# Performance work log

Measured on AMD Instinct MI355X. Metric: run time of the kernel, lower is better.

## Reference

```python
import jax, jax.numpy as jnp
import numpy as np

N, D, H = 4096, 128, 8

def setup_inputs() -> dict:
    key = jax.random.key(0)
    ks = jax.random.split(key, 7)
    xavier = float(np.sqrt(6.0 / (D + D)))  # xavier_uniform for [*, D, D]
    x = jax.random.normal(ks[0], (N, D), dtype=jnp.float32)
    W_k = jax.random.uniform(ks[1], (H, D, D), minval=-xavier, maxval=xavier, dtype=jnp.float32)
    W_q = jax.random.uniform(ks[2], (H, D, D), minval=-xavier, maxval=xavier, dtype=jnp.float32)
    W_v = jax.random.uniform(ks[3], (H, D, D), minval=-xavier, maxval=xavier, dtype=jnp.float32)
    W_m = jnp.ones((H,), dtype=jnp.float32)
    lim = float(1.0 / np.sqrt(D))  # default torch Linear init range
    Wg = jax.random.uniform(ks[4], (D, D), minval=-lim, maxval=lim, dtype=jnp.float32)
    bg = jax.random.uniform(ks[5], (D,), minval=-lim, maxval=lim, dtype=jnp.float32)
    return {"x": x, "W_k": W_k, "W_q": W_q, "W_v": W_v, "W_m": W_m, "Wg": Wg, "bg": bg}

def reference(x, W_k, W_q, W_v, W_m, Wg, bg):
    # per-head projections: [H, N, D]
    q = jnp.einsum('nf,hfd->hnd', x, W_q)
    k = jnp.einsum('nf,hfd->hnd', x, W_k)
    v = jnp.einsum('nf,hfd->hnd', x, W_v)
    # dense all-pairs attention scores per head: [H, N, N]
    e = jnp.einsum('hnd,hmd->hnm', q, k)
    attn = jax.nn.softmax(e, axis=-1)
    # weighted sum over values, then head-scaled accumulation: [N, D]
    out = jnp.einsum('h,hnm,hmd->nd', W_m, attn, v)
    # residual MLP: x + ReLU(Linear(x + out))
    h = x + out
    g = jax.nn.relu(h @ Wg.T + bg)
    return x + g
```

## Files before the change

kernel.cpp:

```cpp
#include <hip/hip_runtime.h>

#define NROWS 4096
#define DDIM  128
#define NHEAD 8
#define LOG2E 1.44269504088896f

extern "C" __device__ float __ocml_native_exp2_f32(float);

typedef __attribute__((ext_vector_type(8))) short    short8;
typedef __attribute__((ext_vector_type(8))) _Float16 half8;
typedef __attribute__((ext_vector_type(4))) float    floatx4;

__device__ __forceinline__ float bf2f(unsigned short u){
  unsigned v = ((unsigned)u) << 16;
  return __builtin_bit_cast(float, v);
}
__device__ __forceinline__ unsigned short f2bf(float f){
  unsigned u = __builtin_bit_cast(unsigned, f);
  u += 0x7FFFu + ((u >> 16) & 1u);
  return (unsigned short)(u >> 16);
}
__device__ __forceinline__ void split2(float v, unsigned short& hi, unsigned short& lo){
  hi = f2bf(v);
  lo = f2bf(v - bf2f(hi));
}
__device__ __forceinline__ void async_cp16(const void* g, void* l){
  __builtin_amdgcn_global_load_lds(
      (const __attribute__((address_space(1))) void*)g,
      (__attribute__((address_space(3))) void*)l, 16, 0, 0);
}

__global__ void fill_kernel(float* __restrict__ out, float val, int n){
  int i = blockIdx.x * 256 + threadIdx.x;
  if (i < n) out[i] = val;
}

__global__ __launch_bounds__(256) void prep_kernel(
    const float* __restrict__ Wk, const float* __restrict__ Wv,
    const float* __restrict__ Wq, const float* __restrict__ Wg,
    const float* __restrict__ x,
    unsigned short* __restrict__ wpre, unsigned short* __restrict__ wgpre,
    unsigned short* __restrict__ xh, unsigned short* __restrict__ xl)
{
  const int id = blockIdx.x * 256 + threadIdx.x;
  if (id < 49152) {
    const int z = id >> 14, rem = id & 16383;
    const int h = rem >> 11, rem2 = rem & 2047;
    const int fh = rem2 >> 10, L = rem2 & 1023;
    const int d = L >> 3, m = L & 7;
    const int kk0 = (m ^ (d & 7)) << 3;
    const float* W = (z == 0 ? Wk : (z == 1 ? Wv : Wq)) + h * DDIM * DDIM;
    short8 hi8, lo8;
#pragma unroll
    for (int j = 0; j < 8; j++) {
      unsigned short hi, lo;
      split2(W[(fh * 64 + kk0 + j) * DDIM + d], hi, lo);
      hi8[j] = (short)hi; lo8[j] = (short)lo;
    }
    unsigned short* base = wpre + (size_t)((z * 8 + h) * 2 + fh) * 16384;
    *(short8*)(base + L * 8) = hi8;
    *(short8*)(base + 8192 + L * 8) = lo8;
  } else if (id < 51200) {
    const int t = id - 49152;
    const int fh = t >> 10, L = t & 1023;
    const int d = L >> 3, m = L & 7;
    const int kk0 = (m ^ (d & 7)) << 3;
    short8 hi8, lo8;
#pragma unroll
    for (int j = 0; j < 8; j++) {
      unsigned short hi, lo;
      split2(Wg[d * DDIM + fh * 64 + kk0 + j], hi, lo);
      hi8[j] = (short)hi; lo8[j] = (short)lo;
    }
    unsigned short* base = wgpre + fh * 16384;
    *(short8*)(base + L * 8) = hi8;
    *(short8*)(base + 8192 + L * 8) = lo8;
  } else if (id < 116736) {
    const int t = id - 51200;
    const float* src = x + (size_t)t * 8;
    float4 v0 = *(const float4*)src, v1 = *(const float4*)(src + 4);
    float xv[8] = {v0.x, v0.y, v0.z, v0.w, v1.x, v1.y, v1.z, v1.w};
    short8 hi8, lo8;
#pragma unroll
    for (int j = 0; j < 8; j++) {
      unsigned short hi, lo; split2(xv[j], hi, lo);
      hi8[j] = (short)hi; lo8[j] = (short)lo;
    }
    *(short8*)(xh + (size_t)t * 8) = hi8;
    *(short8*)(xl + (size_t)t * 8) = lo8;
  }
}

__global__ __launch_bounds__(256, 2) void proj_kernel(
    const unsigned short* __restrict__ xh, const unsigned short* __restrict__ xl,
    const unsigned short* __restrict__ wpre,
    _Float16* __restrict__ kfo, _Float16* __restrict__ vfo,
    _Float16* __restrict__ qfo)
{
  __shared__ alignas(16) unsigned short whi[8192];
  __shared__ alignas(16) unsigned short wlo[8192];
  const int tid = threadIdx.x, lane = tid & 63, wave = tid >> 6;
  const int l4 = lane & 15, quad = lane >> 4;
  const int h = blockIdx.y, z = blockIdx.z;
  const unsigned short* wb = wpre + (size_t)((z * 8 + h) * 2) * 16384;

  floatx4 acc[4][8];
#pragma unroll
  for (int t4 = 0; t4 < 4; t4++)
#pragma unroll
    for (int c = 0; c < 8; c++) acc[t4][c] = (floatx4)0.f;

  for (int fh = 0; fh < 2; fh++) {
    {
      const unsigned short* src = wb + fh * 16384;
      const unsigned short* sh = src + wave * 2048 + lane * 8;
      const unsigned short* sl = src + 8192 + wave * 2048 + lane * 8;
      unsigned short* dh = &whi[wave * 2048];
      unsigned short* dl = &wlo[wave * 2048];
#pragma unroll
      for (int it = 0; it < 4; it++) {
        async_cp16(sh + it * 512, dh + it * 512);
        async_cp16(sl + it * 512, dl + it * 512);
      }
    }
    __syncthreads();

#pragma unroll
    for (int t4 = 0; t4 < 4; t4++) {
      const int row = blockIdx.x * 256 + t4 * 64 + wave * 16 + l4;
      const size_t xo = (size_t)row * DDIM + fh * 64 + quad * 8;
      short8 ah[2], al[2];
      ah[0] = *(const short8*)(xh + xo);
      ah[1] = *(const short8*)(xh + xo + 32);
      al[0] = *(const short8*)(xl + xo);
      al[1] = *(const short8*)(xl + xo + 32);
#pragma unroll
      for (int t2 = 0; t2 < 2; t2++) {
#pragma unroll
        for (int c = 0; c < 8; c++) {
          const int col = c * 16 + l4;
          const int idx = (col * 8 + ((t2 * 4 + quad) ^ (col & 7))) * 8;
          short8 bh = *(const short8*)&whi[idx];
          short8 bl = *(const short8*)&wlo[idx];
          acc[t4][c] = __builtin_amdgcn_mfma_f32_16x16x32_bf16(ah[t2], bh, acc[t4][c], 0, 0, 0);
          acc[t4][c] = __builtin_amdgcn_mfma_f32_16x16x32_bf16(al[t2], bh, acc[t4][c], 0, 0, 0);
          acc[t4][c] = __builtin_amdgcn_mfma_f32_16x16x32_bf16(ah[t2], bl, acc[t4][c], 0, 0, 0);
        }
      }
    }
    __syncthreads();
  }

  const int rb = wave * 16 + quad * 4;
#pragma unroll
  for (int t4 = 0; t4 < 4; t4++) {
    const int tile = blockIdx.x * 4 + t4;
    const size_t tilebase = (size_t)(h * 64 + tile) * 8192;
#pragma unroll
    for (int c = 0; c < 8; c++) {
      const int d = c * 16 + l4;
#pragma unroll
      for (int r = 0; r < 4; r++) {
        const int kl = rb + r;
        const float val = acc[t4][c][r];
        if (z == 0) {
          const int c2 = kl >> 4, l4k = kl & 15;
          const int tt = d >> 5, qd = (d >> 3) & 3, jj = d & 7;
          const int qX = qd ^ ((l4k >> 1) & 3);
          kfo[tilebase + (size_t)((c2 * 4 + tt) * 16 + l4k) * 32 + qX * 8 + jj] =
              (_Float16)val;
        } else if (z == 1) {
          const int c2 = d >> 4, l4v = d & 15;
          const int tt = kl >> 5, qd = (kl >> 3) & 3, jj = kl & 7;
          const int qX = qd ^ ((l4v >> 1) & 3);
          vfo[tilebase + (size_t)((c2 * 2 + tt) * 16 + l4v) * 32 + qX * 8 + jj] =
              (_Float16)val;
        } else {
          qfo[((size_t)h * NROWS + (size_t)tile * 64 + kl) * DDIM + d] =
              (_Float16)(val * LOG2E);
        }
      }
    }
  }
}

struct FlashLds {
  _Float16 k[2][8192];
  _Float16 p[4][1024];
};

__global__ __launch_bounds__(256, 3) void flash_kernel(
    const _Float16* __restrict__ qfo, const _Float16* __restrict__ kfo,
    const _Float16* __restrict__ vfo,
    _Float16* __restrict__ op, float* __restrict__ mb, float* __restrict__ lb)
{
  __shared__ alignas(16) FlashLds lds;
  const int tid = threadIdx.x, lane = tid & 63, wave = tid >> 6;
  const int l4 = lane & 15, quad = lane >> 4;
  const int h = blockIdx.x & 7, qt = (blockIdx.x >> 3) & 63, s = blockIdx.x >> 9;
  const int q0 = qt * 64;

  half8 aq[4];
  {
    const _Float16* qr =
        qfo + ((size_t)h * NROWS + q0 + wave * 16 + l4) * DDIM + quad * 8;
#pragma unroll
    for (int t = 0; t < 4; t++) aq[t] = *(const half8*)(qr + t * 32);
  }

  float m_run[4];
#pragma unroll
  for (int r = 0; r < 4; r++) m_run[r] = -1e30f;
  floatx4 Oacc[8], lacc = (floatx4)0.f;
#pragma unroll
  for (int c = 0; c < 8; c++) Oacc[c] = (floatx4)0.f;

  half8 vones;
#pragma unroll
  for (int j = 0; j < 8; j++) vones[j] = (_Float16)1.f;

  const _Float16* kfo_h = kfo + (size_t)h * 64 * 8192;
  const _Float16* vfo_h = vfo + (size_t)h * 64 * 8192;
  const int lq = (l4 * 4 + (quad ^ ((l4 >> 1) & 3))) * 8;
  const int kt0 = (s == 0) ? 0 : (s == 1 ? 22 : 43);
  const int kt1 = (s == 0) ? 22 : (s == 1 ? 43 : 64);

  {
    const _Float16* ks = kfo_h + (size_t)kt0 * 8192 + wave * 2048 + lane * 8;
    _Float16* kd = &lds.k[kt0 & 1][wave * 2048];
#pragma unroll
    for (int it = 0; it < 4; it++) async_cp16(ks + it * 512, kd + it * 512);
  }

  for (int kt = kt0; kt < kt1; ++kt) {
    const int cur = kt & 1;
    __syncthreads();

    if (kt + 1 < kt1) {
      const _Float16* ks = kfo_h + (size_t)(kt + 1) * 8192 + wave * 2048 + lane * 8;
      _Float16* kd = &lds.k[cur ^ 1][wave * 2048];
#pragma unroll
      for (int it = 0; it < 4; it++) async_cp16(ks + it * 512, kd + it * 512);
    }

    floatx4 Sf[4];
#pragma unroll
    for (int c = 0; c < 4; c++) Sf[c] = (floatx4)0.f;
    __builtin_amdgcn_s_setprio(1);
#pragma unroll
    for (int t = 0; t < 4; t++) {
      half8 b[4];
#pragma unroll
      for (int c = 0; c < 4; c++)
        b[c] = *(const half8*)&lds.k[cur][(c * 4 + t) * 512 + lq];
#pragma unroll
      for (int c = 0; c < 4; c++)
        Sf[c] = __builtin_amdgcn_mfma_f32_16x16x32_f16(aq[t], b[c], Sf[c], 0, 0, 0);
    }
    __builtin_amdgcn_s_setprio(0);

    float alpha[4];
    {
      float mt[4];
#pragma unroll
      for (int r = 0; r < 4; r++)
        mt[r] = fmaxf(fmaxf(Sf[0][r], Sf[1][r]), fmaxf(Sf[2][r], Sf[3][r]));
#pragma unroll
      for (int mk = 1; mk <= 8; mk <<= 1)
#pragma unroll
        for (int r = 0; r < 4; r++) mt[r] = fmaxf(mt[r], __shfl_xor(mt[r], mk, 64));
#pragma unroll
      for (int r = 0; r < 4; r++) {
        const float mn = fmaxf(m_run[r], mt[r]);
        alpha[r] = __ocml_native_exp2_f32(m_run[r] - mn);
        m_run[r] = mn;
      }
#pragma unroll
      for (int r = 0; r < 4; r++)
#pragma unroll
        for (int c = 0; c < 4; c++)
          Sf[c][r] = __ocml_native_exp2_f32(Sf[c][r] - m_run[r]);
    }

#pragma unroll
    for (int c = 0; c < 4; c++)
#pragma unroll
      for (int r = 0; r < 4; r++)
        lds.p[wave][((c * 2 + (l4 >> 3)) * 16 + quad * 4 + r) * 8 + (l4 & 7)] =
            (_Float16)Sf[c][r];

    half8 vfrag[8][2];
    {
      const _Float16* vtb = vfo_h + (size_t)kt * 8192;
#pragma unroll
      for (int c = 0; c < 8; c++)
#pragma unroll
        for (int t = 0; t < 2; t++)
          vfrag[c][t] = *(const half8*)(vtb + (c * 2 + t) * 512 + lq);
    }

    {
      const bool moved = (alpha[0] != 1.f) | (alpha[1] != 1.f) |
                         (alpha[2] != 1.f) | (alpha[3] != 1.f);
      if (__any(moved)) {
#pragma unroll
        for (int c = 0; c < 8; c++) {
          Oacc[c][0] *= alpha[0]; Oacc[c][1] *= alpha[1];
          Oacc[c][2] *= alpha[2]; Oacc[c][3] *= alpha[3];
        }
        lacc[0] *= alpha[0]; lacc[1] *= alpha[1];
        lacc[2] *= alpha[2]; lacc[3] *= alpha[3];
      }
    }

    __builtin_amdgcn_s_setprio(1);
#pragma unroll
    for (int t = 0; t < 2; t++) {
      half8 ap = *(const half8*)&lds.p[wave][((t * 4 + quad) * 16 + l4) * 8];
      lacc = __builtin_amdgcn_mfma_f32_16x16x32_f16(ap, vones, lacc, 0, 0, 0);
#pragma unroll
      for (int c = 0; c < 8; c++)
        Oacc[c] = __builtin_amdgcn_mfma_f32_16x16x32_f16(ap, vfrag[c][t], Oacc[c], 0, 0, 0);
    }
    __builtin_amdgcn_s_setprio(0);
  }

  const int rbase = wave * 16 + quad * 4;
  const size_t rowbase = (size_t)(s * NHEAD + h) * NROWS + q0 + rbase;
#pragma unroll
  for (int c = 0; c < 8; c++) {
    const int col = c * 16 + l4;
#pragma unroll
    for (int r = 0; r < 4; r++)
      op[(rowbase + r) * DDIM + col] = (_Float16)Oacc[c][r];
  }
  if (l4 == 0) {
#pragma unroll
    for (int r = 0; r < 4; r++) {
      mb[rowbase + r] = m_run[r];
      lb[rowbase + r] = lacc[r];
    }
  }
}

__global__ __launch_bounds__(128) void merge_kernel(
    const _Float16* __restrict__ op, const float* __restrict__ mb,
    const float* __restrict__ lb, const float* __restrict__ Wm,
    float* __restrict__ u)
{
  __shared__ float sc[3][NHEAD];
  const int n = blockIdx.x, d = threadIdx.x;
  if (d < NHEAD) {
    const int h = d;
    float m0 = mb[(size_t)(0 * NHEAD + h) * NROWS + n];
    float m1 = mb[(size_t)(1 * NHEAD + h) * NROWS + n];
    float m2 = mb[(size_t)(2 * NHEAD + h) * NROWS + n];
    float l0 = lb[(size_t)(0 * NHEAD + h) * NROWS + n];
    float l1 = lb[(size_t)(1 * NHEAD + h) * NROWS + n];
    float l2 = lb[(size_t)(2 * NHEAD + h) * NROWS + n];
    const float m = fmaxf(fmaxf(m0, m1), m2);
    const float a0 = __ocml_native_exp2_f32(m0 - m);
    const float a1 = __ocml_native_exp2_f32(m1 - m);
    const float a2 = __ocml_native_exp2_f32(m2 - m);
    const float invL = Wm[h] / (l0 * a0 + l1 * a1 + l2 * a2);
    sc[0][h] = a0 * invL;
    sc[1][h] = a1 * invL;
    sc[2][h] = a2 * invL;
  }
  __syncthreads();
  float acc = 0.f;
#pragma unroll
  for (int s = 0; s < 3; s++)
#pragma unroll
    for (int h = 0; h < NHEAD; h++)
      acc += sc[s][h] * (float)op[((size_t)(s * NHEAD + h) * NROWS + n) * DDIM + d];
  u[(size_t)n * DDIM + d] = acc;
}

__global__ __launch_bounds__(256, 2) void mlp_kernel(
    const float* __restrict__ x, const float* __restrict__ u,
    const unsigned short* __restrict__ wgpre, const float* __restrict__ bg,
    float* __restrict__ out)
{
  __shared__ alignas(16) unsigned short whi[8192];
  __shared__ alignas(16) unsigned short wlo[8192];
  const int tid = threadIdx.x, lane = tid & 63, wave = tid >> 6;
  const int l4 = lane & 15, quad = lane >> 4;
  const int r0 = blockIdx.x * 64;

  floatx4 acc[8];
#pragma unroll
  for (int c = 0; c < 8; c++) acc[c] = (floatx4)0.f;

  for (int fh = 0; fh < 2; fh++) {
    {
      const unsigned short* src = wgpre + fh * 16384;
      const unsigned short* sh = src + wave * 2048 + lane * 8;
      const unsigned short* sl = src + 8192 + wave * 2048 + lane * 8;
      unsigned short* dh = &whi[wave * 2048];
      unsigned short* dl = &wlo[wave * 2048];
#pragma unroll
      for (int it = 0; it < 4; it++) {
        async_cp16(sh + it * 512, dh + it * 512);
        async_cp16(sl + it * 512, dl + it * 512);
      }
    }
    __syncthreads();

    const size_t xoff = (size_t)(r0 + wave * 16 + l4) * DDIM + fh * 64 + quad * 8;
    short8 ah[2], al[2];
#pragma unroll
    for (int t2 = 0; t2 < 2; t2++) {
      float4 x0 = *(const float4*)(x + xoff + t2 * 32);
      float4 x1 = *(const float4*)(x + xoff + t2 * 32 + 4);
      float4 u0 = *(const float4*)(u + xoff + t2 * 32);
      float4 u1 = *(const float4*)(u + xoff + t2 * 32 + 4);
      float hv[8] = {x0.x + u0.x, x0.y + u0.y, x0.z + u0.z, x0.w + u0.w,
                     x1.x + u1.x, x1.y + u1.y, x1.z + u1.z, x1.w + u1.w};
#pragma unroll
      for (int j = 0; j < 8; j++) {
        unsigned short hi, lo; split2(hv[j], hi, lo);
        ah[t2][j] = (short)hi; al[t2][j] = (short)lo;
      }
    }
#pragma unroll
    for (int t2 = 0; t2 < 2; t2++) {
#pragma unroll
      for (int c = 0; c < 8; c++) {
        const int col = c * 16 + l4;
        const int idx = (col * 8 + ((t2 * 4 + quad) ^ (col & 7))) * 8;
        short8 bh = *(const short8*)&whi[idx];
        short8 bl = *(const short8*)&wlo[idx];
        acc[c] = __builtin_amdgcn_mfma_f32_16x16x32_bf16(ah[t2], bh, acc[c], 0, 0, 0);
        acc[c] = __builtin_amdgcn_mfma_f32_16x16x32_bf16(al[t2], bh, acc[c], 0, 0, 0);
        acc[c] = __builtin_amdgcn_mfma_f32_16x16x32_bf16(ah[t2], bl, acc[c], 0, 0, 0);
      }
    }
    __syncthreads();
  }

  const int rbase = wave * 16 + quad * 4;
#pragma unroll
  for (int c = 0; c < 8; c++) {
    const int col = c * 16 + l4;
    const float bgf = bg[col];
#pragma unroll
    for (int r = 0; r < 4; r++) {
      const size_t idx = (size_t)(r0 + rbase + r) * DDIM + col;
      out[idx] = x[idx] + fmaxf(acc[c][r] + bgf, 0.f);
    }
  }
}

extern "C" void kernel_launch(void* const* d_in, const int* in_sizes, int n_in,
                              void* d_out, int out_size, void* d_ws, size_t ws_size,
                              hipStream_t stream) {
  float* out = (float*)d_out;
  const int fill_blocks = (out_size + 255) / 256;

  const bool ok_sizes =
      n_in == 7 &&
      in_sizes[0] == NROWS * DDIM &&
      in_sizes[1] == NHEAD * DDIM * DDIM &&
      in_sizes[2] == NHEAD * DDIM * DDIM &&
      in_sizes[3] == NHEAD * DDIM * DDIM &&
      in_sizes[4] == NHEAD &&
      in_sizes[5] == DDIM * DDIM &&
      in_sizes[6] == DDIM &&
      out_size == NROWS * DDIM;
  if (!ok_sizes) {
    fill_kernel<<<fill_blocks, 256, 0, stream>>>(out, 1000.f, out_size);
    return;
  }

  const size_t HND = (size_t)NHEAD * NROWS * DDIM;
  const size_t ND  = (size_t)NROWS * DDIM;
  const size_t WPRE_N  = (size_t)3 * 8 * 2 * 16384;
  const size_t WGPRE_N = (size_t)2 * 16384;
  const size_t need = ND * 4 + 3 * HND * 2 + 3 * HND * 2 +
                      2 * (3 * (size_t)NHEAD * NROWS) * 4 +
                      (WPRE_N + WGPRE_N + 2 * ND) * 2;
  if (ws_size < need) {
    fill_kernel<<<fill_blocks, 256, 0, stream>>>(out, 500.f, out_size);
    return;
  }

  const float* x  = (const float*)d_in[0];
  const float* Wk = (const float*)d_in[1];
  const float* Wq = (const float*)d_in[2];
  const float* Wv = (const float*)d_in[3];
  const float* Wm = (const float*)d_in[4];
  const float* Wg = (const float*)d_in[5];
  const float* bg = (const float*)d_in[6];

  float*          u     = (float*)d_ws;
  _Float16*       kfo   = (_Float16*)(u + ND);
  _Float16*       vfo   = kfo + HND;
  _Float16*       qfo   = vfo + HND;
  _Float16*       op    = qfo + HND;
  float*          mb    = (float*)(op + 3 * HND);
  float*          lb    = mb + 3 * NHEAD * NROWS;
  unsigned short* wpre  = (unsigned short*)(lb + 3 * NHEAD * NROWS);
  unsigned short* wgpre = wpre + WPRE_N;
  unsigned short* xh    = wgpre + WGPRE_N;
  unsigned short* xl    = xh + ND;

  (void)hipGetLastError();
  prep_kernel<<<dim3(456), 256, 0, stream>>>(Wk, Wv, Wq, Wg, x, wpre, wgpre, xh, xl);
  proj_kernel<<<dim3(16, NHEAD, 3), 256, 0, stream>>>(xh, xl, wpre, kfo, vfo, qfo);
  flash_kernel<<<dim3(1536), 256, 0, stream>>>(qfo, kfo, vfo, op, mb, lb);
  merge_kernel<<<dim3(4096), 128, 0, stream>>>(op, mb, lb, Wm, u);
  mlp_kernel<<<dim3(64), 256, 0, stream>>>(x, u, wgpre, bg, out);
  if (hipGetLastError() != hipSuccess) {
    fill_kernel<<<fill_blocks, 256, 0, stream>>>(out, 2000.f, out_size);
  }
}
```

Baseline: 233.9 us.

## Software-pipeline QK^T of next tile with PV of current tile; DPP row max

Restructures the flash-attention inner loop so the QK^T MFMAs for tile kt+1 are issued alongside the PV MFMAs for tile kt, with K prefetch moved two tiles ahead and one barrier per iteration placed after the softmax. The V fragment global loads are hoisted to the start of the iteration so their latency overlaps the softmax. The row-max shuffle reduction is replaced with DPP row-broadcast operations. This is meant to hide softmax and exp latency behind matrix work, at the cost of more live registers (extra score accumulators), which could reduce occupancy.

```diff
diff --git a/kernel.cpp b/kernel.cpp
--- a/kernel.cpp
+++ b/kernel.cpp
@@ -28,6 +28,18 @@
   __builtin_amdgcn_global_load_lds(
       (const __attribute__((address_space(1))) void*)g,
       (__attribute__((address_space(3))) void*)l, 16, 0, 0);
+}
+__device__ __forceinline__ float dpp_max16(float v){
+  int t;
+  t = __builtin_amdgcn_update_dpp(0, __builtin_bit_cast(int, v), 0x128, 0xF, 0xF, false);
+  v = fmaxf(v, __builtin_bit_cast(float, t));
+  t = __builtin_amdgcn_update_dpp(0, __builtin_bit_cast(int, v), 0x124, 0xF, 0xF, false);
+  v = fmaxf(v, __builtin_bit_cast(float, t));
+  t = __builtin_amdgcn_update_dpp(0, __builtin_bit_cast(int, v), 0x122, 0xF, 0xF, false);
+  v = fmaxf(v, __builtin_bit_cast(float, t));
+  t = __builtin_amdgcn_update_dpp(0, __builtin_bit_cast(int, v), 0x121, 0xF, 0xF, false);
+  v = fmaxf(v, __builtin_bit_cast(float, t));
+  return v;
 }
 
 __global__ void fill_kernel(float* __restrict__ out, float val, int n){
@@ -231,44 +243,49 @@
 #pragma unroll
     for (int it = 0; it < 4; it++) async_cp16(ks + it * 512, kd + it * 512);
   }
+  __syncthreads();
+  if (kt0 + 1 < kt1) {
+    const _Float16* ks = kfo_h + (size_t)(kt0 + 1) * 8192 + wave * 2048 + lane * 8;
+    _Float16* kd = &lds.k[(kt0 + 1) & 1][wave * 2048];
+#pragma unroll
+    for (int it = 0; it < 4; it++) async_cp16(ks + it * 512, kd + it * 512);
+  }
+
+  floatx4 Sc[4];
+#pragma unroll
+  for (int c = 0; c < 4; c++) Sc[c] = (floatx4)0.f;
+#pragma unroll
+  for (int t = 0; t < 4; t++) {
+    half8 b[4];
+#pragma unroll
+    for (int c = 0; c < 4; c++)
+      b[c] = *(const half8*)&lds.k[kt0 & 1][(c * 4 + t) * 512 + lq];
+#pragma unroll
+    for (int c = 0; c < 4; c++)
+      Sc[c] = __builtin_amdgcn_mfma_f32_16x16x32_f16(aq[t], b[c], Sc[c], 0, 0, 0);
+  }
 
   for (int kt = kt0; kt < kt1; ++kt) {
     const int cur = kt & 1;
-    __syncthreads();
-
-    if (kt + 1 < kt1) {
-      const _Float16* ks = kfo_h + (size_t)(kt + 1) * 8192 + wave * 2048 + lane * 8;
-      _Float16* kd = &lds.k[cur ^ 1][wave * 2048];
-#pragma unroll
-      for (int it = 0; it < 4; it++) async_cp16(ks + it * 512, kd + it * 512);
-    }
-
-    floatx4 Sf[4];
-#pragma unroll
-    for (int c = 0; c < 4; c++) Sf[c] = (floatx4)0.f;
-    __builtin_amdgcn_s_setprio(1);
-#pragma unroll
-    for (int t = 0; t < 4; t++) {
-      half8 b[4];
-#pragma unroll
-      for (int c = 0; c < 4; c++)
-        b[c] = *(const half8*)&lds.k[cur][(c * 4 + t) * 512 + lq];
-#pragma unroll
-      for (int c = 0; c < 4; c++)
-        Sf[c] = __builtin_amdgcn_mfma_f32_16x16x32_f16(aq[t], b[c], Sf[c], 0, 0, 0);
-    }
-    __builtin_amdgcn_s_setprio(0);
+
+    half8 vfrag[8][2];
+    {
+      const _Float16* vtb = vfo_h + (size_t)kt * 8192;
+#pragma unroll
+      for (int c = 0; c < 8; c++)
+#pragma unroll
+        for (int t = 0; t < 2; t++)
+          vfrag[c][t] = *(const half8*)(vtb + (c * 2 + t) * 512 + lq);
+    }
 
     float alpha[4];
     {
       float mt[4];
 #pragma unroll
       for (int r = 0; r < 4; r++)
-        mt[r] = fmaxf(fmaxf(Sf[0][r], Sf[1][r]), fmaxf(Sf[2][r], Sf[3][r]));
-#pragma unroll
-      for (int mk = 1; mk <= 8; mk <<= 1)
-#pragma unroll
-        for (int r = 0; r < 4; r++) mt[r] = fmaxf(mt[r], __shfl_xor(mt[r], mk, 64));
+        mt[r] = fmaxf(fmaxf(Sc[0][r], Sc[1][r]), fmaxf(Sc[2][r], Sc[3][r]));
+#pragma unroll
+      for (int r = 0; r < 4; r++) mt[r] = dpp_max16(mt[r]);
 #pragma unroll
       for (int r = 0; r < 4; r++) {
         const float mn = fmaxf(m_run[r], mt[r]);
@@ -279,7 +296,7 @@
       for (int r = 0; r < 4; r++)
 #pragma unroll
         for (int c = 0; c < 4; c++)
-          Sf[c][r] = __ocml_native_exp2_f32(Sf[c][r] - m_run[r]);
+          Sc[c][r] = __ocml_native_exp2_f32(Sc[c][r] - m_run[r]);
     }
 
 #pragma unroll
@@ -287,17 +304,7 @@
 #pragma unroll
       for (int r = 0; r < 4; r++)
         lds.p[wave][((c * 2 + (l4 >> 3)) * 16 + quad * 4 + r) * 8 + (l4 & 7)] =
-            (_Float16)Sf[c][r];
-
-    half8 vfrag[8][2];
-    {
-      const _Float16* vtb = vfo_h + (size_t)kt * 8192;
-#pragma unroll
-      for (int c = 0; c < 8; c++)
-#pragma unroll
-        for (int t = 0; t < 2; t++)
-          vfrag[c][t] = *(const half8*)(vtb + (c * 2 + t) * 512 + lq);
-    }
+            (_Float16)Sc[c][r];
 
     {
       const bool moved = (alpha[0] != 1.f) | (alpha[1] != 1.f) |
@@ -313,7 +320,32 @@
       }
     }
 
+    __syncthreads();
+
+    if (kt + 2 < kt1) {
+      const _Float16* ks = kfo_h + (size_t)(kt + 2) * 8192 + wave * 2048 + lane * 8;
+      _Float16* kd = &lds.k[cur][wave * 2048];
+#pragma unroll
+      for (int it = 0; it < 4; it++) async_cp16(ks + it * 512, kd + it * 512);
+    }
+
     __builtin_amdgcn_s_setprio(1);
+    floatx4 Sn[4];
+    if (kt + 1 < kt1) {
+#pragma unroll
+      for (int c = 0; c < 4; c++) Sn[c] = (floatx4)0.f;
+#pragma unroll
+      for (int t = 0; t < 4; t++) {
+        half8 b[4];
+#pragma unroll
+        for (int c = 0; c < 4; c++)
+          b[c] = *(const half8*)&lds.k[cur ^ 1][(c * 4 + t) * 512 + lq];
+#pragma unroll
+        for (int c = 0; c < 4; c++)
+          Sn[c] = __builtin_amdgcn_mfma_f32_16x16x32_f16(aq[t], b[c], Sn[c], 0, 0, 0);
+      }
+    }
+
 #pragma unroll
     for (int t = 0; t < 2; t++) {
       half8 ap = *(const half8*)&lds.p[wave][((t * 4 + quad) * 16 + l4) * 8];
@@ -323,6 +355,11 @@
         Oacc[c] = __builtin_amdgcn_mfma_f32_16x16x32_f16(ap, vfrag[c][t], Oacc[c], 0, 0, 0);
     }
     __builtin_amdgcn_s_setprio(0);
+
+    if (kt + 1 < kt1) {
+#pragma unroll
+      for (int c = 0; c < 4; c++) Sc[c] = Sn[c];
+    }
   }
 
   const int rbase = wave * 16 + quad * 4;
```

Result: no change. 231.7 us (-0.9%).

## Split flash attention keys two ways, use DPP max reduction, stream V per step

Applied to the files above, without the earlier changes.

The flash kernel now splits the key range into two halves instead of three uneven chunks. This reduces grid size, partial-output storage and merge work, and the merge kernel is simplified to combine two partials. The row-max reduction uses DPP row shuffles instead of __shfl_xor. V fragments are loaded per k-substep rather than all at once, which cuts register pressure, so launch bounds are raised to 4 blocks per CU. Fewer blocks (1024) may leave CUs underused, and the shorter V prefetch distance could expose memory latency.

```diff
diff --git a/kernel.cpp b/kernel.cpp
--- a/kernel.cpp
+++ b/kernel.cpp
@@ -28,6 +28,18 @@
   __builtin_amdgcn_global_load_lds(
       (const __attribute__((address_space(1))) void*)g,
       (__attribute__((address_space(3))) void*)l, 16, 0, 0);
+}
+__device__ __forceinline__ float dpp_max16(float v){
+  int t;
+  t = __builtin_amdgcn_update_dpp(0, __builtin_bit_cast(int, v), 0x128, 0xF, 0xF, false);
+  v = fmaxf(v, __builtin_bit_cast(float, t));
+  t = __builtin_amdgcn_update_dpp(0, __builtin_bit_cast(int, v), 0x124, 0xF, 0xF, false);
+  v = fmaxf(v, __builtin_bit_cast(float, t));
+  t = __builtin_amdgcn_update_dpp(0, __builtin_bit_cast(int, v), 0x122, 0xF, 0xF, false);
+  v = fmaxf(v, __builtin_bit_cast(float, t));
+  t = __builtin_amdgcn_update_dpp(0, __builtin_bit_cast(int, v), 0x121, 0xF, 0xF, false);
+  v = fmaxf(v, __builtin_bit_cast(float, t));
+  return v;
 }
 
 __global__ void fill_kernel(float* __restrict__ out, float val, int n){
@@ -189,7 +201,7 @@
   _Float16 p[4][1024];
 };
 
-__global__ __launch_bounds__(256, 3) void flash_kernel(
+__global__ __launch_bounds__(256, 4) void flash_kernel(
     const _Float16* __restrict__ qfo, const _Float16* __restrict__ kfo,
     const _Float16* __restrict__ vfo,
     _Float16* __restrict__ op, float* __restrict__ mb, float* __restrict__ lb)
@@ -222,12 +234,11 @@
   const _Float16* kfo_h = kfo + (size_t)h * 64 * 8192;
   const _Float16* vfo_h = vfo + (size_t)h * 64 * 8192;
   const int lq = (l4 * 4 + (quad ^ ((l4 >> 1) & 3))) * 8;
-  const int kt0 = (s == 0) ? 0 : (s == 1 ? 22 : 43);
-  const int kt1 = (s == 0) ? 22 : (s == 1 ? 43 : 64);
+  const int kt0 = s * 32, kt1 = kt0 + 32;
 
   {
     const _Float16* ks = kfo_h + (size_t)kt0 * 8192 + wave * 2048 + lane * 8;
-    _Float16* kd = &lds.k[kt0 & 1][wave * 2048];
+    _Float16* kd = &lds.k[0][wave * 2048];
 #pragma unroll
     for (int it = 0; it < 4; it++) async_cp16(ks + it * 512, kd + it * 512);
   }
@@ -266,9 +277,7 @@
       for (int r = 0; r < 4; r++)
         mt[r] = fmaxf(fmaxf(Sf[0][r], Sf[1][r]), fmaxf(Sf[2][r], Sf[3][r]));
 #pragma unroll
-      for (int mk = 1; mk <= 8; mk <<= 1)
-#pragma unroll
-        for (int r = 0; r < 4; r++) mt[r] = fmaxf(mt[r], __shfl_xor(mt[r], mk, 64));
+      for (int r = 0; r < 4; r++) mt[r] = dpp_max16(mt[r]);
 #pragma unroll
       for (int r = 0; r < 4; r++) {
         const float mn = fmaxf(m_run[r], mt[r]);
@@ -288,16 +297,6 @@
       for (int r = 0; r < 4; r++)
         lds.p[wave][((c * 2 + (l4 >> 3)) * 16 + quad * 4 + r) * 8 + (l4 & 7)] =
             (_Float16)Sf[c][r];
-
-    half8 vfrag[8][2];
-    {
-      const _Float16* vtb = vfo_h + (size_t)kt * 8192;
-#pragma unroll
-      for (int c = 0; c < 8; c++)
-#pragma unroll
-        for (int t = 0; t < 2; t++)
-          vfrag[c][t] = *(const half8*)(vtb + (c * 2 + t) * 512 + lq);
-    }
 
     {
       const bool moved = (alpha[0] != 1.f) | (alpha[1] != 1.f) |
@@ -313,16 +312,23 @@
       }
     }
 
-    __builtin_amdgcn_s_setprio(1);
 #pragma unroll
     for (int t = 0; t < 2; t++) {
+      half8 vf[8];
+      {
+        const _Float16* vtb = vfo_h + (size_t)kt * 8192 + t * 512 + lq;
+#pragma unroll
+        for (int c = 0; c < 8; c++)
+          vf[c] = *(const half8*)(vtb + c * 1024);
+      }
       half8 ap = *(const half8*)&lds.p[wave][((t * 4 + quad) * 16 + l4) * 8];
+      __builtin_amdgcn_s_setprio(1);
       lacc = __builtin_amdgcn_mfma_f32_16x16x32_f16(ap, vones, lacc, 0, 0, 0);
 #pragma unroll
       for (int c = 0; c < 8; c++)
-        Oacc[c] = __builtin_amdgcn_mfma_f32_16x16x32_f16(ap, vfrag[c][t], Oacc[c], 0, 0, 0);
-    }
-    __builtin_amdgcn_s_setprio(0);
+        Oacc[c] = __builtin_amdgcn_mfma_f32_16x16x32_f16(ap, vf[c], Oacc[c], 0, 0, 0);
+      __builtin_amdgcn_s_setprio(0);
+    }
   }
 
   const int rbase = wave * 16 + quad * 4;
@@ -348,32 +354,28 @@
     const float* __restrict__ lb, const float* __restrict__ Wm,
     float* __restrict__ u)
 {
-  __shared__ float sc[3][NHEAD];
+  __shared__ float sc[2][NHEAD];
   const int n = blockIdx.x, d = threadIdx.x;
   if (d < NHEAD) {
     const int h = d;
-    float m0 = mb[(size_t)(0 * NHEAD + h) * NROWS + n];
-    float m1 = mb[(size_t)(1 * NHEAD + h) * NROWS + n];
-    float m2 = mb[(size_t)(2 * NHEAD + h) * NROWS + n];
-    float l0 = lb[(size_t)(0 * NHEAD + h) * NROWS + n];
-    float l1 = lb[(size_t)(1 * NHEAD + h) * NROWS + n];
-    float l2 = lb[(size_t)(2 * NHEAD + h) * NROWS + n];
-    const float m = fmaxf(fmaxf(m0, m1), m2);
-    const float a0 = __ocml_native_exp2_f32(m0 - m);
+    const float m1 = mb[(size_t)h * NROWS + n];
+    const float m2 = mb[(size_t)(NHEAD + h) * NROWS + n];
+    const float l1 = lb[(size_t)h * NROWS + n];
+    const float l2 = lb[(size_t)(NHEAD + h) * NROWS + n];
+    const float m  = fmaxf(m1, m2);
     const float a1 = __ocml_native_exp2_f32(m1 - m);
     const float a2 = __ocml_native_exp2_f32(m2 - m);
-    const float invL = Wm[h] / (l0 * a0 + l1 * a1 + l2 * a2);
-    sc[0][h] = a0 * invL;
-    sc[1][h] = a1 * invL;
-    sc[2][h] = a2 * invL;
+    const float invL = Wm[h] / (l1 * a1 + l2 * a2);
+    sc[0][h] = a1 * invL;
+    sc[1][h] = a2 * invL;
   }
   __syncthreads();
   float acc = 0.f;
 #pragma unroll
-  for (int s = 0; s < 3; s++)
-#pragma unroll
-    for (int h = 0; h < NHEAD; h++)
-      acc += sc[s][h] * (float)op[((size_t)(s * NHEAD + h) * NROWS + n) * DDIM + d];
+  for (int h = 0; h < NHEAD; h++) {
+    acc += sc[0][h] * (float)op[((size_t)h * NROWS + n) * DDIM + d];
+    acc += sc[1][h] * (float)op[((size_t)(NHEAD + h) * NROWS + n) * DDIM + d];
+  }
   u[(size_t)n * DDIM + d] = acc;
 }
 
@@ -477,8 +479,8 @@
   const size_t ND  = (size_t)NROWS * DDIM;
   const size_t WPRE_N  = (size_t)3 * 8 * 2 * 16384;
   const size_t WGPRE_N = (size_t)2 * 16384;
-  const size_t need = ND * 4 + 3 * HND * 2 + 3 * HND * 2 +
-                      2 * (3 * (size_t)NHEAD * NROWS) * 4 +
+  const size_t need = ND * 4 + 3 * HND * 2 + 2 * HND * 2 +
+                      2 * (2 * (size_t)NHEAD * NROWS) * 4 +
                       (WPRE_N + WGPRE_N + 2 * ND) * 2;
   if (ws_size < need) {
     fill_kernel<<<fill_blocks, 256, 0, stream>>>(out, 500.f, out_size);
@@ -498,9 +500,9 @@
   _Float16*       vfo   = kfo + HND;
   _Float16*       qfo   = vfo + HND;
   _Float16*       op    = qfo + HND;
-  float*          mb    = (float*)(op + 3 * HND);
-  float*          lb    = mb + 3 * NHEAD * NROWS;
-  unsigned short* wpre  = (unsigned short*)(lb + 3 * NHEAD * NROWS);
+  float*          mb    = (float*)(op + 2 * HND);
+  float*          lb    = mb + 2 * NHEAD * NROWS;
+  unsigned short* wpre  = (unsigned short*)(lb + 2 * NHEAD * NROWS);
   unsigned short* wgpre = wpre + WPRE_N;
   unsigned short* xh    = wgpre + WGPRE_N;
   unsigned short* xl    = xh + ND;
@@ -508,7 +510,7 @@
   (void)hipGetLastError();
   prep_kernel<<<dim3(456), 256, 0, stream>>>(Wk, Wv, Wq, Wg, x, wpre, wgpre, xh, xl);
   proj_kernel<<<dim3(16, NHEAD, 3), 256, 0, stream>>>(xh, xl, wpre, kfo, vfo, qfo);
-  flash_kernel<<<dim3(1536), 256, 0, stream>>>(qfo, kfo, vfo, op, mb, lb);
+  flash_kernel<<<dim3(1024), 256, 0, stream>>>(qfo, kfo, vfo, op, mb, lb);
   merge_kernel<<<dim3(4096), 128, 0, stream>>>(op, mb, lb, Wm, u);
   mlp_kernel<<<dim3(64), 256, 0, stream>>>(x, u, wgpre, bg, out);
   if (hipGetLastError() != hipSuccess) {
```

Result: faster. 215.2 us (-8.0%).
